# Optimization experiments

Measured on AMD Instinct MI355X. Metric: run time of the kernel, lower is better.

The kernel has to match this reference:

```python
import jax, jax.numpy as jnp
import numpy as np

B, L, DIN, D = 16, 1024, 512, 1024  # batch, l_max, input_dim, d_model
ORDER = 2


def setup_inputs() -> dict:
    key = jax.random.key(0)
    ks = jax.random.split(key, 8)
    n = lambda i, shape, sc: jax.random.normal(ks[i], shape, dtype=jnp.float32) * sc
    return {
        "x": n(0, (B, L, DIN), 1.0),
        # project_in (Linear since input_dim != output_dim)
        "Wp": n(1, (DIN, D), DIN ** -0.5),
        "bp": jnp.zeros((D,), jnp.float32),
        # hyena in_proj -> (order+1)*d channels
        "W_in": n(2, (D, 3 * D), D ** -0.5),
        "b_in": jnp.zeros((3 * D,), jnp.float32),
        # depthwise causal short conv, kernel 3
        "short_w": n(3, (3 * D, 1, 3), 0.5),
        "short_b": jnp.zeros((3 * D,), jnp.float32),
        # implicit long filters (materialized) + per-channel skip bias
        "k_filt": n(4, (ORDER, L, D), 0.02),
        "D_bias": n(5, (ORDER, D), 1.0),
        # hyena out_proj
        "W_out": n(6, (D, D), D ** -0.5),
        "b_out": jnp.zeros((D,), jnp.float32),
    }


def _fftconv(v, k, d_bias):
    # v: [B, L, d], k: [L, d] -> causal long conv via zero-padded FFT + skip
    n = 2 * v.shape[1]
    vf = jnp.fft.rfft(v.astype(jnp.float32), n=n, axis=1)
    kf = jnp.fft.rfft(k.astype(jnp.float32), n=n, axis=0)
    y = jnp.fft.irfft(vf * kf[None], n=n, axis=1)[:, : v.shape[1]]
    return (y + v * d_bias).astype(v.dtype)


def reference(x, Wp, bp, W_in, b_in, short_w, short_b, k_filt, D_bias, W_out, b_out):
    u = x @ Wp + bp                      # [B, L, D] project_in
    u = u @ W_in + b_in                  # [B, L, 3D]
    # depthwise causal short conv over sequence
    uc = jnp.transpose(u, (0, 2, 1))     # [B, 3D, L]
    uc = jax.lax.conv_general_dilated(
        uc, short_w, window_strides=(1,), padding=[(2, 0)],
        feature_group_count=3 * D, dimension_numbers=("NCH", "OIH", "NCH"),
    )[..., :L] + short_b[None, :, None]
    uc = jnp.transpose(uc, (0, 2, 1))    # [B, L, 3D]
    x1, x2, v = jnp.split(uc, 3, axis=-1)
    # Hyena recurrence: gate then long FFT conv, order=2
    v = _fftconv(v * x2, k_filt[0], D_bias[0])
    v = _fftconv(v * x1, k_filt[1], D_bias[1])
    return v @ W_out + b_out             # [B, L, D]
```

## Files before the change

### kernel.cpp

```cpp
#include <hip/hip_runtime.h>

#define BATCH 16
#define LSEQ 1024
#define DIN 512
#define DMODEL 1024
#define D3 3072
#define KCP 1064

typedef __attribute__((ext_vector_type(4))) float f32x4;
typedef __attribute__((ext_vector_type(8))) short bf16x8;

static __device__ __forceinline__ ushort f2bf(float f) {
    uint u = __float_as_uint(f);
    return (ushort)((u + 0x7FFFu + ((u >> 16) & 1u)) >> 16);
}
static __device__ __forceinline__ float bf2f(ushort h) {
    return __uint_as_float(((uint)h) << 16);
}

#define GLD16(ldst, gsrc)                                                        \
    __builtin_amdgcn_global_load_lds(                                            \
        (const __attribute__((address_space(1))) void*)(gsrc),                   \
        (__attribute__((address_space(3))) void*)(ldst), 16, 0, 0)

template <typename OutT, bool HAS_BIAS>
__global__ __launch_bounds__(512) void gemm_mfma(const ushort* __restrict__ A,
                                                 const ushort* __restrict__ Bt,
                                                 const float* __restrict__ bias,
                                                 OutT* __restrict__ C,
                                                 int M, int N, int K) {
    __shared__ ushort Als[2][256 * 32];
    __shared__ ushort Bls[2][128 * 32];
    int nwg = gridDim.x * gridDim.y;
    int bid = blockIdx.y * gridDim.x + blockIdx.x;
    bid = (bid & 7) * (nwg >> 3) + (bid >> 3);
    int n0 = (bid % gridDim.x) * 128, m0 = (bid / gridDim.x) * 256;
    int t = threadIdx.x;
    int w = t >> 6, l = t & 63;
    int wm = w >> 1, wn = w & 1;
    f32x4 acc[4][4] = {};

    int arow0 = 32 * w + (l >> 2);
    int kpart = (l & 3) * 8;
    const ushort* gA0 = A + (size_t)(m0 + arow0) * K + kpart;
    const ushort* gA1 = gA0 + (size_t)16 * K;
    const ushort* gB0 = Bt + (size_t)(n0 + 16 * w + (l >> 2)) * K + kpart;
    int soA = 1024 * w;
    int soB = 512 * w;

    int aoff = (wm * 64 + (l & 15)) * 32 + (l >> 4) * 8;
    int boff = (wn * 64 + (l & 15)) * 32 + (l >> 4) * 8;

    GLD16(&Als[0][soA], gA0);
    GLD16(&Als[0][soA + 512], gA1);
    GLD16(&Bls[0][soB], gB0);
    GLD16(&Als[1][soA], gA0 + 32);
    GLD16(&Als[1][soA + 512], gA1 + 32);
    GLD16(&Bls[1][soB], gB0 + 32);

    int cur = 0;
    for (int k0 = 0; k0 < K; k0 += 32) {
        if (k0 + 32 < K)
            asm volatile("s_waitcnt vmcnt(3)" ::: "memory");
        else
            asm volatile("s_waitcnt vmcnt(0)" ::: "memory");
        __builtin_amdgcn_s_barrier();
        __builtin_amdgcn_sched_barrier(0);
        bf16x8 af[4], bg[4];
#pragma unroll
        for (int i = 0; i < 4; i++) af[i] = *(const bf16x8*)&Als[cur][aoff + i * 512];
#pragma unroll
        for (int j = 0; j < 4; j++) bg[j] = *(const bf16x8*)&Bls[cur][boff + j * 512];
#pragma unroll
        for (int i = 0; i < 4; i++)
#pragma unroll
            for (int j = 0; j < 4; j++)
                acc[i][j] = __builtin_amdgcn_mfma_f32_16x16x32_bf16(af[i], bg[j],
                                                                    acc[i][j], 0, 0, 0);
        asm volatile("s_waitcnt lgkmcnt(0)" ::: "memory");
        __builtin_amdgcn_sched_barrier(0);
        __builtin_amdgcn_s_barrier();
        if (k0 + 64 < K) {
            GLD16(&Als[cur][soA], gA0 + k0 + 64);
            GLD16(&Als[cur][soA + 512], gA1 + k0 + 64);
            GLD16(&Bls[cur][soB], gB0 + k0 + 64);
        }
        cur ^= 1;
    }

#pragma unroll
    for (int j = 0; j < 4; j++) {
        int col = n0 + wn * 64 + 16 * j + (l & 15);
        float bv = HAS_BIAS ? bias[col] : 0.f;
#pragma unroll
        for (int i = 0; i < 4; i++) {
            int row0 = m0 + wm * 64 + 16 * i + (l >> 4) * 4;
#pragma unroll
            for (int r = 0; r < 4; r++) {
                float v = acc[i][j][r] + bv;
                if constexpr (sizeof(OutT) == 2)
                    C[(size_t)(row0 + r) * N + col] = (OutT)f2bf(v);
                else
                    C[(size_t)(row0 + r) * N + col] = (OutT)v;
            }
        }
    }
}

__global__ __launch_bounds__(512, 2) void conv_mfma(const ushort* __restrict__ At,
                                                    const ushort* __restrict__ X1t,
                                                    const float* __restrict__ kt,
                                                    const float* __restrict__ Db,
                                                    ushort* __restrict__ V2t, int nb) {
    __shared__ ushort a_lds[16 * 1024];
    __shared__ ushort kc[8 * KCP];
    int d = blockIdx.x;
    int tid = threadIdx.x;
    int w = tid >> 6, l = tid & 63;
    int lr = l & 15, lq = l >> 4;

    {
        int b = tid >> 5, s = tid & 31;
        const ushort* g = At + ((size_t)b * DMODEL + d) * LSEQ + s * 32;
#pragma unroll
        for (int j = 0; j < 4; j++) {
            uint4 v = {0u, 0u, 0u, 0u};
            if (b < nb) v = *(const uint4*)(g + 8 * j);
            int byte = (b * 1024 + s * 32 + 8 * j) * 2;
            *(uint4*)((char*)a_lds + (byte ^ (b << 4))) = v;
        }
    }

    int p = (7 - lr) & 7;
    int v0 = 1023 - lr + 8 * lq - p;
    int a_base = lr * 2048 + lq * 16;
    int swz = lr << 4;
    const int tis[4] = {w, 31 - w, 8 + w, 23 - w};
    int ti0 = tis[0], ti1 = tis[1], ti2 = tis[2], ti3 = tis[3];

    ushort gpre[4][2][4];
#pragma unroll
    for (int ii = 0; ii < 4; ii++)
#pragma unroll
        for (int h = 0; h < 2; h++)
#pragma unroll
            for (int r = 0; r < 4; r++) {
                int b = lq * 4 + r;
                int t2 = 32 * tis[ii] + 16 * h + lr;
                gpre[ii][h][r] = (b < nb)
                    ? X1t[((size_t)b * DMODEL + d) * LSEQ + t2] : (ushort)0;
            }

    for (int o = 0; o < 2; o++) {
        const float* krow = kt + ((size_t)o * DMODEL + d) * LSEQ;
        for (int idx = tid; idx < 8 * KCP; idx += 512) {
            int pp = idx / KCP;
            int u = idx - pp * KCP;
            int ki = 1023 - u - pp;
            kc[idx] = f2bf((ki >= 0) ? krow[ki] : 0.f);
        }
        __syncthreads();

        f32x4 a00 = {}, a01 = {}, a10 = {}, a11 = {};
        f32x4 a20 = {}, a21 = {}, a30 = {}, a31 = {};
        const char* kbp = (const char*)kc + ((size_t)p * KCP + v0) * 2;
        for (int m = 0; m < 32; m++) {
            bf16x8 b0 = *(const bf16x8*)(kbp - 64 * m);
            bf16x8 b1 = *(const bf16x8*)(kbp - 64 * m - 32);
            __builtin_amdgcn_s_setprio(1);
#define CSTEP(TI, A0, A1)                                                      \
            if ((TI) >= m) {                                                   \
                bf16x8 af = *(const bf16x8*)((const char*)a_lds +              \
                                             ((a_base + 64 * ((TI) - m)) ^ swz)); \
                A0 = __builtin_amdgcn_mfma_f32_16x16x32_bf16(af, b0, A0, 0, 0, 0); \
                A1 = __builtin_amdgcn_mfma_f32_16x16x32_bf16(af, b1, A1, 0, 0, 0); \
            }
            CSTEP(ti0, a00, a01)
            CSTEP(ti1, a10, a11)
            CSTEP(ti2, a20, a21)
            CSTEP(ti3, a30, a31)
#undef CSTEP
            __builtin_amdgcn_s_setprio(0);
        }
        float db = Db[o * DMODEL + d];
        __syncthreads();
#define CEPI(II, TI, AC, H)                                                    \
        {                                                                      \
            _Pragma("unroll")                                                  \
            for (int r = 0; r < 4; r++) {                                      \
                int t2 = 32 * (TI) + 16 * (H) + lr;                            \
                int b = lq * 4 + r;                                            \
                int ab = ((b * 1024 + t2) * 2) ^ (b << 4);                     \
                float a0v = bf2f(*(const ushort*)((const char*)a_lds + ab));   \
                float y = (AC)[r] + a0v * db;                                  \
                if (o == 0) y *= bf2f(gpre[II][H][r]);                         \
                *(ushort*)((char*)a_lds + ab) = f2bf(y);                       \
            }                                                                  \
        }
        CEPI(0, ti0, a00, 0) CEPI(0, ti0, a01, 1)
        CEPI(1, ti1, a10, 0) CEPI(1, ti1, a11, 1)
        CEPI(2, ti2, a20, 0) CEPI(2, ti2, a21, 1)
        CEPI(3, ti3, a30, 0) CEPI(3, ti3, a31, 1)
#undef CEPI
    }
    __syncthreads();
    {
        int b = tid >> 5, s = tid & 31;
        if (b < nb) {
            ushort* g = V2t + ((size_t)b * DMODEL + d) * LSEQ + s * 32;
#pragma unroll
            for (int j = 0; j < 4; j++) {
                int byte = (b * 1024 + s * 32 + 8 * j) * 2;
                uint4 v = *(const uint4*)((const char*)a_lds + (byte ^ (b << 4)));
                *(uint4*)(g + 8 * j) = v;
            }
        }
    }
}

__global__ void cvt_bf16(const float* __restrict__ in, ushort* __restrict__ out, int n4) {
    int i = blockIdx.x * blockDim.x + threadIdx.x;
    if (i >= n4) return;
    float4 v = *(const float4*)&in[4 * i];
    uint2 pk;
    pk.x = (uint)f2bf(v.x) | ((uint)f2bf(v.y) << 16);
    pk.y = (uint)f2bf(v.z) | ((uint)f2bf(v.w) << 16);
    *(uint2*)&out[4 * i] = pk;
}

__global__ void transpose_cvt(const float* __restrict__ in, ushort* __restrict__ out,
                              int R, int C) {
    __shared__ float tile[32][33];
    int c0 = blockIdx.x * 32, r0 = blockIdx.y * 32;
    int tx = threadIdx.x, ty = threadIdx.y;
#pragma unroll
    for (int i = 0; i < 4; i++)
        tile[ty + 8 * i][tx] = in[(size_t)(r0 + ty + 8 * i) * C + c0 + tx];
    __syncthreads();
#pragma unroll
    for (int i = 0; i < 4; i++)
        out[(size_t)(c0 + ty + 8 * i) * R + r0 + tx] = f2bf(tile[tx][ty + 8 * i]);
}

__global__ __launch_bounds__(256) void transpose_b16(const ushort* __restrict__ in,
                                                     ushort* __restrict__ out) {
    __shared__ uint tile[64][33];
    int t0 = blockIdx.x * 64, d0 = blockIdx.y * 64, b = blockIdx.z;
    int i = threadIdx.x;
    const ushort* ip = in + (size_t)b * DMODEL * LSEQ;
    ushort* op = out + (size_t)b * LSEQ * DMODEL;
    int dl = i >> 5, cu = i & 31;
#pragma unroll
    for (int j = 0; j < 8; j++)
        tile[dl + 8 * j][cu] =
            *(const uint*)&ip[(size_t)(d0 + dl + 8 * j) * LSEQ + t0 + 2 * cu];
    __syncthreads();
    int du = i & 31, tb = i >> 5;
#pragma unroll
    for (int j = 0; j < 8; j++) {
        int tl = tb + 8 * j;
        uint lo = (tile[2 * du][tl >> 1] >> (16 * (tl & 1))) & 0xFFFFu;
        uint hi = (tile[2 * du + 1][tl >> 1] >> (16 * (tl & 1))) & 0xFFFFu;
        *(uint*)&op[(size_t)(t0 + tl) * DMODEL + d0 + 2 * du] = lo | (hi << 16);
    }
}

__global__ void bias_fuse(const float* __restrict__ bp, const float* __restrict__ W_in,
                          const float* __restrict__ b_in, float* __restrict__ bf) {
    int n = blockIdx.x * blockDim.x + threadIdx.x;
    float s = b_in[n];
    for (int k = 0; k < DMODEL; k++) s += bp[k] * W_in[(size_t)k * D3 + n];
    bf[n] = s;
}

__global__ void transpose_k(const float* __restrict__ kf, float* __restrict__ kt) {
    __shared__ float tile[32][33];
    int s0 = blockIdx.x * 32, d0 = blockIdx.y * 32, o = blockIdx.z;
    int tx = threadIdx.x, ty = threadIdx.y;
#pragma unroll
    for (int i = 0; i < 4; i++)
        tile[ty + 8 * i][tx] = kf[((size_t)o * LSEQ + s0 + ty + 8 * i) * DMODEL + d0 + tx];
    __syncthreads();
#pragma unroll
    for (int i = 0; i < 4; i++)
        kt[((size_t)o * DMODEL + d0 + ty + 8 * i) * LSEQ + s0 + tx] = tile[tx][ty + 8 * i];
}

__global__ __launch_bounds__(256) void shortconv_gate(const ushort* __restrict__ UC,
                                                      const float* __restrict__ sw,
                                                      const float* __restrict__ sb,
                                                      ushort* __restrict__ At,
                                                      ushort* __restrict__ X1t) {
    __shared__ uint tin[34][33];
    __shared__ ushort oA[64][34];
    __shared__ ushort oX[64][34];
    int t0 = blockIdx.x * 32, c0 = blockIdx.y * 64, b = blockIdx.z;
    int tx = threadIdx.x, ty = threadIdx.y;
    float2 res[3][4];
#pragma unroll
    for (int g = 0; g < 3; g++) {
        int ch = g * DMODEL + c0 + 2 * tx;
        __syncthreads();
        for (int r = ty; r < 34; r += 8) {
            int t = t0 + r - 2;
            tin[r][tx] = (t >= 0)
                ? *(const uint*)&UC[((size_t)b * LSEQ + t) * D3 + ch] : 0u;
        }
        __syncthreads();
        float w00 = sw[ch * 3 + 0], w01 = sw[ch * 3 + 1], w02 = sw[ch * 3 + 2];
        float w10 = sw[ch * 3 + 3], w11 = sw[ch * 3 + 4], w12 = sw[ch * 3 + 5];
        float bb0 = sb[ch], bb1 = sb[ch + 1];
#pragma unroll
        for (int i = 0; i < 4; i++) {
            int r = ty + 8 * i + 2;
            uint u0 = tin[r - 2][tx], u1 = tin[r - 1][tx], u2 = tin[r][tx];
            res[g][i].x = w00 * bf2f((ushort)u0) + w01 * bf2f((ushort)u1) +
                          w02 * bf2f((ushort)u2) + bb0;
            res[g][i].y = w10 * bf2f((ushort)(u0 >> 16)) + w11 * bf2f((ushort)(u1 >> 16)) +
                          w12 * bf2f((ushort)(u2 >> 16)) + bb1;
        }
    }
#pragma unroll
    for (int i = 0; i < 4; i++) {
        int t = ty + 8 * i;
        oA[2 * tx][t]     = f2bf(res[2][i].x * res[1][i].x);
        oA[2 * tx + 1][t] = f2bf(res[2][i].y * res[1][i].y);
        oX[2 * tx][t]     = f2bf(res[0][i].x);
        oX[2 * tx + 1][t] = f2bf(res[0][i].y);
    }
    __syncthreads();
    int li = ty * 32 + tx;
    int row = li >> 2, cu0 = (li & 3) * 4;
    ushort* gA = At  + ((size_t)b * DMODEL + c0 + row) * LSEQ + t0;
    ushort* gX = X1t + ((size_t)b * DMODEL + c0 + row) * LSEQ + t0;
#pragma unroll
    for (int j = 0; j < 4; j++) {
        int cu = cu0 + j;
        uint av = (uint)oA[row][2 * cu] | ((uint)oA[row][2 * cu + 1] << 16);
        uint xv = (uint)oX[row][2 * cu] | ((uint)oX[row][2 * cu + 1] << 16);
        *(uint*)&gA[2 * cu] = av;
        *(uint*)&gX[2 * cu] = xv;
    }
}

extern "C" void kernel_launch(void* const* d_in, const int* in_sizes, int n_in,
                              void* d_out, int out_size, void* d_ws, size_t ws_size,
                              hipStream_t stream) {
    (void)in_sizes; (void)n_in; (void)out_size;
    const float* x    = (const float*)d_in[0];
    const float* Wp   = (const float*)d_in[1];
    const float* bp   = (const float*)d_in[2];
    const float* W_in = (const float*)d_in[3];
    const float* b_in = (const float*)d_in[4];
    const float* sw   = (const float*)d_in[5];
    const float* sb   = (const float*)d_in[6];
    const float* kf   = (const float*)d_in[7];
    const float* Db   = (const float*)d_in[8];
    const float* Wout = (const float*)d_in[9];
    const float* bout = (const float*)d_in[10];
    float* out = (float*)d_out;

    char* ws = (char*)d_ws;
    ushort* Wf_t   = (ushort*)(ws);
    float*  bfv    = (float*)(ws + 3145728);
    float*  kt     = (float*)(ws + 3162112);
    ushort* Wout_t = (ushort*)(ws + 11550720);
    const size_t PB = 13647872;

    const size_t XB  = 1048576;
    const size_t ATB = 2097152;
    const size_t X1B = 2097152;
    const size_t UCB = 6291456;
    const size_t V2B = 2097152;
    const size_t PREPB = 7340032;

    int cb = 1, cf = 1;
    {
        bool ok = false;
        for (int tcb = 16; tcb >= 1 && !ok; tcb >>= 1) {
            for (int tcf = tcb; tcf >= 1; tcf >>= 1) {
                size_t ucreg = (size_t)tcf * UCB;
                size_t v2need = (size_t)2 * tcb * V2B;
                if (ucreg < v2need) ucreg = v2need;
                if (ucreg < PREPB) ucreg = PREPB;
                size_t need = PB + (size_t)tcb * (XB + ATB + X1B) + ucreg;
                if (need <= ws_size) { cb = tcb; cf = tcf; ok = true; break; }
            }
        }
    }

    ushort* x_bf = (ushort*)(ws + PB);
    ushort* Atb  = (ushort*)(ws + PB + (size_t)cb * XB);
    ushort* X1tb = (ushort*)(ws + PB + (size_t)cb * (XB + ATB));
    char*   ucrg = ws + PB + (size_t)cb * (XB + ATB + X1B);
    ushort* UC   = (ushort*)ucrg;
    ushort* V2t  = (ushort*)ucrg;
    ushort* V2   = (ushort*)(ucrg + (size_t)cb * V2B);
    ushort* W_inT = (ushort*)ucrg;
    ushort* Wp_bf = (ushort*)(ucrg + 6291456);

    transpose_cvt<<<dim3(96, 32), dim3(32, 8), 0, stream>>>(W_in, W_inT, DMODEL, D3);
    cvt_bf16<<<512, 256, 0, stream>>>(Wp, Wp_bf, DIN * DMODEL / 4);
    gemm_mfma<ushort, false><<<dim3(4, 12), 512, 0, stream>>>(W_inT, Wp_bf, nullptr,
                                                              Wf_t, D3, DIN, DMODEL);
    bias_fuse<<<D3 / 256, 256, 0, stream>>>(bp, W_in, b_in, bfv);
    transpose_cvt<<<dim3(32, 32), dim3(32, 8), 0, stream>>>(Wout, Wout_t, DMODEL, DMODEL);
    transpose_k<<<dim3(32, 32, 2), dim3(32, 8), 0, stream>>>(kf, kt);

    for (int b0 = 0; b0 < BATCH; b0 += cb) {
        cvt_bf16<<<cb * LSEQ * DIN / 1024, 256, 0, stream>>>(
            x + (size_t)b0 * LSEQ * DIN, x_bf, cb * LSEQ * DIN / 4);
        for (int f0 = 0; f0 < cb; f0 += cf) {
            gemm_mfma<ushort, true><<<dim3(24, cf * 4), 512, 0, stream>>>(
                x_bf + (size_t)f0 * LSEQ * DIN, Wf_t, bfv, UC, cf * LSEQ, D3, DIN);
            shortconv_gate<<<dim3(32, 16, cf), dim3(32, 8), 0, stream>>>(
                UC, sw, sb, Atb + (size_t)f0 * DMODEL * LSEQ,
                X1tb + (size_t)f0 * DMODEL * LSEQ);
        }
        conv_mfma<<<DMODEL, 512, 0, stream>>>(Atb, X1tb, kt, Db, V2t, cb);
        transpose_b16<<<dim3(16, 16, cb), dim3(256), 0, stream>>>(V2t, V2);
        gemm_mfma<float, true><<<dim3(8, cb * 4), 512, 0, stream>>>(
            V2, Wout_t, bout, out + (size_t)b0 * LSEQ * DMODEL, cb * LSEQ, DMODEL, DMODEL);
    }
}
```

Baseline: 409.5 us.

## Triple-buffer GEMM LDS pipeline, split bias fusion, batch shortconv loads

The GEMM mainloop moves from two to three LDS stages, so each k-tile is prefetched two iterations ahead, with vmcnt waits adjusted to match. The serial 1024-step bias fusion kernel becomes a partial-sum kernel split over 8 k-chunks plus a small reduction kernel. The short-conv gate kernel now loads all three channel groups into separate shared tiles under a single barrier instead of syncing per group. The extra LDS per block (48KB to 72KB in the GEMM) may lower occupancy, and the bias split needs extra workspace.

After: 342.2 us. 1.2x faster.

```diff
diff --git a/kernel.cpp b/kernel.cpp
--- a/kernel.cpp
+++ b/kernel.cpp
@@ -29,8 +29,8 @@
                                                  const float* __restrict__ bias,
                                                  OutT* __restrict__ C,
                                                  int M, int N, int K) {
-    __shared__ ushort Als[2][256 * 32];
-    __shared__ ushort Bls[2][128 * 32];
+    __shared__ ushort Als[3][256 * 32];
+    __shared__ ushort Bls[3][128 * 32];
     int nwg = gridDim.x * gridDim.y;
     int bid = blockIdx.y * gridDim.x + blockIdx.x;
     bid = (bid & 7) * (nwg >> 3) + (bid >> 3);
@@ -51,16 +51,19 @@
     int aoff = (wm * 64 + (l & 15)) * 32 + (l >> 4) * 8;
     int boff = (wn * 64 + (l & 15)) * 32 + (l >> 4) * 8;
 
-    GLD16(&Als[0][soA], gA0);
-    GLD16(&Als[0][soA + 512], gA1);
-    GLD16(&Bls[0][soB], gB0);
-    GLD16(&Als[1][soA], gA0 + 32);
-    GLD16(&Als[1][soA + 512], gA1 + 32);
-    GLD16(&Bls[1][soB], gB0 + 32);
+#pragma unroll
+    for (int s = 0; s < 3; s++) {
+        GLD16(&Als[s][soA], gA0 + 32 * s);
+        GLD16(&Als[s][soA + 512], gA1 + 32 * s);
+        GLD16(&Bls[s][soB], gB0 + 32 * s);
+    }
 
     int cur = 0;
     for (int k0 = 0; k0 < K; k0 += 32) {
-        if (k0 + 32 < K)
+        int rem = (K - k0 - 32) >> 5;
+        if (rem >= 2)
+            asm volatile("s_waitcnt vmcnt(6)" ::: "memory");
+        else if (rem == 1)
             asm volatile("s_waitcnt vmcnt(3)" ::: "memory");
         else
             asm volatile("s_waitcnt vmcnt(0)" ::: "memory");
@@ -80,12 +83,12 @@
         asm volatile("s_waitcnt lgkmcnt(0)" ::: "memory");
         __builtin_amdgcn_sched_barrier(0);
         __builtin_amdgcn_s_barrier();
-        if (k0 + 64 < K) {
-            GLD16(&Als[cur][soA], gA0 + k0 + 64);
-            GLD16(&Als[cur][soA + 512], gA1 + k0 + 64);
-            GLD16(&Bls[cur][soB], gB0 + k0 + 64);
-        }
-        cur ^= 1;
+        if (k0 + 96 < K) {
+            GLD16(&Als[cur][soA], gA0 + k0 + 96);
+            GLD16(&Als[cur][soA + 512], gA1 + k0 + 96);
+            GLD16(&Bls[cur][soB], gB0 + k0 + 96);
+        }
+        cur = (cur == 2) ? 0 : cur + 1;
     }
 
 #pragma unroll
@@ -265,11 +268,22 @@
     }
 }
 
-__global__ void bias_fuse(const float* __restrict__ bp, const float* __restrict__ W_in,
-                          const float* __restrict__ b_in, float* __restrict__ bf) {
-    int n = blockIdx.x * blockDim.x + threadIdx.x;
+__global__ void bias_fuse_part(const float* __restrict__ bp,
+                               const float* __restrict__ W_in,
+                               float* __restrict__ partial) {
+    int n = blockIdx.x * 256 + threadIdx.x;
+    int k0 = blockIdx.y * 128;
+    float s = 0.f;
+    for (int k = k0; k < k0 + 128; k++) s += bp[k] * W_in[(size_t)k * D3 + n];
+    partial[(size_t)blockIdx.y * D3 + n] = s;
+}
+__global__ void bias_fuse_red(const float* __restrict__ partial,
+                              const float* __restrict__ b_in,
+                              float* __restrict__ bf) {
+    int n = blockIdx.x * 256 + threadIdx.x;
     float s = b_in[n];
-    for (int k = 0; k < DMODEL; k++) s += bp[k] * W_in[(size_t)k * D3 + n];
+#pragma unroll
+    for (int j = 0; j < 8; j++) s += partial[(size_t)j * D3 + n];
     bf[n] = s;
 }
 
@@ -291,29 +305,32 @@
                                                       const float* __restrict__ sb,
                                                       ushort* __restrict__ At,
                                                       ushort* __restrict__ X1t) {
-    __shared__ uint tin[34][33];
+    __shared__ uint tin[3][34][33];
     __shared__ ushort oA[64][34];
     __shared__ ushort oX[64][34];
     int t0 = blockIdx.x * 32, c0 = blockIdx.y * 64, b = blockIdx.z;
     int tx = threadIdx.x, ty = threadIdx.y;
-    float2 res[3][4];
 #pragma unroll
     for (int g = 0; g < 3; g++) {
         int ch = g * DMODEL + c0 + 2 * tx;
-        __syncthreads();
         for (int r = ty; r < 34; r += 8) {
             int t = t0 + r - 2;
-            tin[r][tx] = (t >= 0)
+            tin[g][r][tx] = (t >= 0)
                 ? *(const uint*)&UC[((size_t)b * LSEQ + t) * D3 + ch] : 0u;
         }
-        __syncthreads();
+    }
+    __syncthreads();
+    float2 res[3][4];
+#pragma unroll
+    for (int g = 0; g < 3; g++) {
+        int ch = g * DMODEL + c0 + 2 * tx;
         float w00 = sw[ch * 3 + 0], w01 = sw[ch * 3 + 1], w02 = sw[ch * 3 + 2];
         float w10 = sw[ch * 3 + 3], w11 = sw[ch * 3 + 4], w12 = sw[ch * 3 + 5];
         float bb0 = sb[ch], bb1 = sb[ch + 1];
 #pragma unroll
         for (int i = 0; i < 4; i++) {
             int r = ty + 8 * i + 2;
-            uint u0 = tin[r - 2][tx], u1 = tin[r - 1][tx], u2 = tin[r][tx];
+            uint u0 = tin[g][r - 2][tx], u1 = tin[g][r - 1][tx], u2 = tin[g][r][tx];
             res[g][i].x = w00 * bf2f((ushort)u0) + w01 * bf2f((ushort)u1) +
                           w02 * bf2f((ushort)u2) + bb0;
             res[g][i].y = w10 * bf2f((ushort)(u0 >> 16)) + w11 * bf2f((ushort)(u1 >> 16)) +
@@ -372,7 +389,7 @@
     const size_t X1B = 2097152;
     const size_t UCB = 6291456;
     const size_t V2B = 2097152;
-    const size_t PREPB = 7340032;
+    const size_t PREPB = 7471104;
 
     int cb = 1, cf = 1;
     {
@@ -398,12 +415,14 @@
     ushort* V2   = (ushort*)(ucrg + (size_t)cb * V2B);
     ushort* W_inT = (ushort*)ucrg;
     ushort* Wp_bf = (ushort*)(ucrg + 6291456);
+    float*  bfp   = (float*)(ucrg + 7340032);
 
     transpose_cvt<<<dim3(96, 32), dim3(32, 8), 0, stream>>>(W_in, W_inT, DMODEL, D3);
     cvt_bf16<<<512, 256, 0, stream>>>(Wp, Wp_bf, DIN * DMODEL / 4);
     gemm_mfma<ushort, false><<<dim3(4, 12), 512, 0, stream>>>(W_inT, Wp_bf, nullptr,
                                                               Wf_t, D3, DIN, DMODEL);
-    bias_fuse<<<D3 / 256, 256, 0, stream>>>(bp, W_in, b_in, bfv);
+    bias_fuse_part<<<dim3(12, 8), 256, 0, stream>>>(bp, W_in, bfp);
+    bias_fuse_red<<<12, 256, 0, stream>>>(bfp, b_in, bfv);
     transpose_cvt<<<dim3(32, 32), dim3(32, 8), 0, stream>>>(Wout, Wout_t, DMODEL, DMODEL);
     transpose_k<<<dim3(32, 32, 2), dim3(32, 8), 0, stream>>>(kf, kt);
 
```
